# Kernel tuning notes

Hardware: AMD Instinct MI355X
Metric: run time of the kernel (lower is better)

Reference implementation:

```python
import jax, jax.numpy as jnp
import numpy as np

N = 100000
E = 1600000
D_IN = 128
D_H = 128
BN_EPS = 1e-5


def setup_inputs() -> dict:
    key = jax.random.key(0)
    ks = jax.random.split(key, 8)
    x = jax.random.normal(ks[0], (N, D_IN), dtype=jnp.float32)
    edge_index = jax.random.randint(ks[1], (2, E), 0, N, dtype=jnp.int64)
    # MLP params (Linear stores weight as [out, in])
    lim1 = 1.0 / np.sqrt(D_IN)
    W1 = jax.random.uniform(ks[2], (D_H, D_IN), minval=-lim1, maxval=lim1, dtype=jnp.float32)
    b1 = jax.random.uniform(ks[3], (D_H,), minval=-lim1, maxval=lim1, dtype=jnp.float32)
    gamma = jnp.ones((D_H,), dtype=jnp.float32)
    beta = jnp.zeros((D_H,), dtype=jnp.float32)
    lim2 = 1.0 / np.sqrt(D_H)
    W2 = jax.random.uniform(ks[4], (D_H, D_H), minval=-lim2, maxval=lim2, dtype=jnp.float32)
    b2 = jax.random.uniform(ks[5], (D_H,), minval=-lim2, maxval=lim2, dtype=jnp.float32)
    eps = jnp.float32(0.0)  # trainable eps parameter, init 0
    return {"x": x, "edge_index": edge_index, "eps": eps, "W1": W1, "b1": b1,
            "gamma": gamma, "beta": beta, "W2": W2, "b2": b2}


def reference(x, edge_index, eps, W1, b1, gamma, beta, W2, b2):
    src = edge_index[0]
    dst = edge_index[1]
    # Augmented edges = original + reversed + self-loops.
    # aggr[dst] += x[src]; aggr[src] += x[dst]; aggr[i] += x[i]
    aggr = jnp.zeros_like(x).at[dst].add(x[src]).at[src].add(x[dst]) + x
    h = (1.0 + eps) * x + aggr              # [N, D_IN]
    h = h @ W1.T + b1                        # [N, D_H]
    # BatchNorm1d in training mode: batch stats, biased variance
    mean = jnp.mean(h, axis=0)
    var = jnp.mean(jnp.square(h - mean), axis=0)
    h = gamma * (h - mean) * jax.lax.rsqrt(var + BN_EPS) + beta
    h = jax.nn.relu(h)
    return h @ W2.T + b2                     # [N, D_H]
```

## Files before the change

kernel.cpp:

```cpp
#include <hip/hip_runtime.h>
#include <hip/hip_fp16.h>

#define N_NODES 100000
#define EDGES   1600000
#define D       128
#define BN_EPS  1e-5f
#define TM      64
#define NT      ((N_NODES + TM - 1) / TM)
#define GGRID   782
#define NB      ((N_NODES + 255) >> 8)
#define SLOT    9216
#define L1E     8
#define L1TILE  (256 * L1E)
#define GBLKS   1536
#define GWAVES  (GBLKS * 4)
#define NREP    32

typedef __attribute__((ext_vector_type(8))) short short8;
typedef __attribute__((ext_vector_type(4))) float f32x4;

__device__ __forceinline__ unsigned short bf_hi(float f) {
    unsigned u = __float_as_uint(f);
    unsigned t = u + 0x7FFF + ((u >> 16) & 1);
    return (unsigned short)(t >> 16);
}
__device__ __forceinline__ float bf_val(unsigned short h) {
    return __uint_as_float(((unsigned)h) << 16);
}

__global__ void zero_split(int* __restrict__ zbase,
                           const float* __restrict__ W1, const float* __restrict__ W2,
                           unsigned short* __restrict__ w1h, unsigned short* __restrict__ w1l,
                           unsigned short* __restrict__ w2h, unsigned short* __restrict__ w2l) {
    int gid = blockIdx.x * blockDim.x + threadIdx.x;
    if (gid < 8704) zbase[gid] = 0;
    if (gid < 16384) {
        float f = W1[gid];
        unsigned short h = bf_hi(f);
        w1h[gid] = h;
        w1l[gid] = bf_hi(f - bf_val(h));
    } else {
        int j = gid - 16384;
        float f = W2[j];
        unsigned short h = bf_hi(f);
        w2h[j] = h;
        w2l[j] = bf_hi(f - bf_val(h));
    }
}

__launch_bounds__(256)
__global__ void partition_pairs(const int* __restrict__ ei, int* __restrict__ gcur,
                                int* __restrict__ pairs) {
    __shared__ int cnt[NB];
    __shared__ int cbase[NB];
    const int tid = threadIdx.x;
    for (int i = tid; i < NB; i += 256) cnt[i] = 0;
    __syncthreads();

    int bbA[L1E], rrA[L1E], pkA[L1E];
    int bbB[L1E], rrB[L1E], pkB[L1E];
    const int t0 = blockIdx.x * L1TILE + tid;
#pragma unroll
    for (int j = 0; j < L1E; ++j) {
        int t = t0 + j * 256;
        bbA[j] = -1;
        bbB[j] = -1;
        if (t < EDGES) {
            int s = ei[t];
            int d = ei[EDGES + t];
            bbA[j] = d >> 8;
            pkA[j] = ((d & 255) << 17) | s;
            rrA[j] = atomicAdd(&cnt[bbA[j]], 1);
            bbB[j] = s >> 8;
            pkB[j] = ((s & 255) << 17) | d;
            rrB[j] = atomicAdd(&cnt[bbB[j]], 1);
        }
    }
    __syncthreads();
    for (int i = tid; i < NB; i += 256) {
        int c = cnt[i];
        cbase[i] = c ? (i * SLOT + atomicAdd(&gcur[i], c)) : 0;
    }
    __syncthreads();
#pragma unroll
    for (int j = 0; j < L1E; ++j) {
        if (bbA[j] >= 0) {
            pairs[cbase[bbA[j]] + rrA[j]] = pkA[j];
            pairs[cbase[bbB[j]] + rrB[j]] = pkB[j];
        }
    }
}

__launch_bounds__(256)
__global__ void bucket_fill(int* __restrict__ pairs, const int* __restrict__ gcur,
                            int* __restrict__ ofs, int* __restrict__ oen) {
    __shared__ int sP[SLOT];
    __shared__ int lc[256];
    __shared__ int cur[256];
    const int b    = blockIdx.x;
    const int tid  = threadIdx.x;
    const int base = b * SLOT;
    const int m    = min(gcur[b], SLOT);
    for (int i = tid; i < m; i += 256) sP[i] = pairs[base + i];
    lc[tid] = 0;
    __syncthreads();
    for (int i = tid; i < m; i += 256) atomicAdd(&lc[sP[i] >> 17], 1);
    __syncthreads();
    int v = lc[tid];
    for (int d = 1; d < 256; d <<= 1) {
        int u = (tid >= d) ? lc[tid - d] : 0;
        __syncthreads();
        lc[tid] += u;
        __syncthreads();
    }
    int abs0 = base + lc[tid] - v;
    cur[tid] = abs0;
    const int n = (b << 8) + tid;
    if (n < N_NODES) { ofs[n] = abs0; oen[n] = abs0 + v; }
    __syncthreads();
    for (int i = tid; i < m; i += 256) {
        int p = sP[i];
        int r = atomicAdd(&cur[p >> 17], 1);
        pairs[r] = p & 0x1FFFF;
    }
}

__launch_bounds__(256)
__global__ void gemm0_mfma(const float* __restrict__ x,
                           const unsigned short* __restrict__ w1h,
                           const unsigned short* __restrict__ w1l,
                           __half* __restrict__ yh) {
    __shared__ unsigned short sH[TM][136];
    __shared__ unsigned short sL[TM][136];
    const int tid = threadIdx.x;
    const int wv  = tid >> 6;
    const int ln  = tid & 63;
    const int lc  = ln & 15;
    const int qd  = ln >> 4;
    const int sr  = tid >> 5;
    const int sc4 = tid & 31;

    short8 Bh[4][2], Bl[4][2];
#pragma unroll
    for (int kk = 0; kk < 4; ++kk)
#pragma unroll
        for (int tl = 0; tl < 2; ++tl) {
            int woff = (wv * 32 + tl * 16 + lc) * D + kk * 32 + qd * 8;
            Bh[kk][tl] = *(const short8*)(w1h + woff);
            Bl[kk][tl] = *(const short8*)(w1l + woff);
        }

    float4 pf[8];
    int tile = blockIdx.x;
#pragma unroll
    for (int i = 0; i < 8; ++i) {
        int gr = tile * TM + sr + i * 8;
        pf[i] = make_float4(0.f, 0.f, 0.f, 0.f);
        if (gr < N_NODES)
            pf[i] = *(const float4*)(x + (long long)gr * D + sc4 * 4);
    }

    while (tile < NT) {
#pragma unroll
        for (int i = 0; i < 8; ++i) {
            float4 v = pf[i];
            unsigned short h0 = bf_hi(v.x), h1b = bf_hi(v.y), h2 = bf_hi(v.z), h3 = bf_hi(v.w);
            unsigned short l0 = bf_hi(v.x - bf_val(h0)), l1 = bf_hi(v.y - bf_val(h1b));
            unsigned short l2 = bf_hi(v.z - bf_val(h2)), l3 = bf_hi(v.w - bf_val(h3));
            int r = sr + i * 8;
            *(uint2*)&sH[r][sc4 * 4] = make_uint2((unsigned)h0 | ((unsigned)h1b << 16),
                                                  (unsigned)h2 | ((unsigned)h3 << 16));
            *(uint2*)&sL[r][sc4 * 4] = make_uint2((unsigned)l0 | ((unsigned)l1 << 16),
                                                  (unsigned)l2 | ((unsigned)l3 << 16));
        }
        __syncthreads();
        int nxt = tile + GGRID;
        if (nxt < NT) {
#pragma unroll
            for (int i = 0; i < 8; ++i) {
                int gr = nxt * TM + sr + i * 8;
                pf[i] = make_float4(0.f, 0.f, 0.f, 0.f);
                if (gr < N_NODES)
                    pf[i] = *(const float4*)(x + (long long)gr * D + sc4 * 4);
            }
        }

        f32x4 acc[4][2];
#pragma unroll
        for (int m = 0; m < 4; ++m)
#pragma unroll
            for (int tl = 0; tl < 2; ++tl) acc[m][tl] = (f32x4){0.f, 0.f, 0.f, 0.f};

#pragma unroll
        for (int kk = 0; kk < 4; ++kk) {
#pragma unroll
            for (int m = 0; m < 4; ++m) {
                short8 ah = *(const short8*)&sH[m * 16 + lc][kk * 32 + qd * 8];
                short8 al = *(const short8*)&sL[m * 16 + lc][kk * 32 + qd * 8];
#pragma unroll
                for (int tl = 0; tl < 2; ++tl) {
                    acc[m][tl] = __builtin_amdgcn_mfma_f32_16x16x32_bf16(ah, Bh[kk][tl], acc[m][tl], 0, 0, 0);
                    acc[m][tl] = __builtin_amdgcn_mfma_f32_16x16x32_bf16(al, Bh[kk][tl], acc[m][tl], 0, 0, 0);
                    acc[m][tl] = __builtin_amdgcn_mfma_f32_16x16x32_bf16(ah, Bl[kk][tl], acc[m][tl], 0, 0, 0);
                }
            }
        }

        const int row0 = tile * TM;
#pragma unroll
        for (int m = 0; m < 4; ++m)
#pragma unroll
            for (int tl = 0; tl < 2; ++tl) {
                int col = wv * 32 + tl * 16 + lc;
#pragma unroll
                for (int r = 0; r < 4; ++r) {
                    int grow = row0 + m * 16 + qd * 4 + r;
                    if (grow < N_NODES)
                        yh[(long long)grow * D + col] = __float2half(acc[m][tl][r]);
                }
            }
        __syncthreads();
        tile = nxt;
    }
}

__launch_bounds__(256)
__global__ void gather_aggr(const __half* __restrict__ yh,
                            const int* __restrict__ adj, const int* __restrict__ ofs,
                            const int* __restrict__ oen, const float* __restrict__ eps_p,
                            const float* __restrict__ b1,
                            float* __restrict__ h1, float* __restrict__ stats) {
    const int wv   = threadIdx.x >> 6;
    const int lane = threadIdx.x & 63;
    const int wave = blockIdx.x * 4 + wv;
    const __half2* xp = (const __half2*)yh;
    const float sc = 2.0f + eps_p[0];
    const float2 b1c = ((const float2*)b1)[lane];
    float sx = 0.f, sy = 0.f, qx = 0.f, qy = 0.f;

    for (int node = wave; node < N_NODES; node += GWAVES) {
        int b = ofs[node];
        int e = oen[node];
        float ax = 0.f, ay = 0.f;
        int i = b;
        for (; i + 8 <= e; i += 8) {
            int n0 = adj[i],     n1 = adj[i + 1], n2 = adj[i + 2], n3 = adj[i + 3];
            int n4 = adj[i + 4], n5 = adj[i + 5], n6 = adj[i + 6], n7 = adj[i + 7];
            __half2 v0 = xp[(unsigned)n0 * 64u + lane];
            __half2 v1 = xp[(unsigned)n1 * 64u + lane];
            __half2 v2 = xp[(unsigned)n2 * 64u + lane];
            __half2 v3 = xp[(unsigned)n3 * 64u + lane];
            __half2 v4 = xp[(unsigned)n4 * 64u + lane];
            __half2 v5 = xp[(unsigned)n5 * 64u + lane];
            __half2 v6 = xp[(unsigned)n6 * 64u + lane];
            __half2 v7 = xp[(unsigned)n7 * 64u + lane];
            float2 f0 = __half22float2(v0);
            float2 f1 = __half22float2(v1);
            float2 f2 = __half22float2(v2);
            float2 f3 = __half22float2(v3);
            float2 f4 = __half22float2(v4);
            float2 f5 = __half22float2(v5);
            float2 f6 = __half22float2(v6);
            float2 f7 = __half22float2(v7);
            ax += ((f0.x + f1.x) + (f2.x + f3.x)) + ((f4.x + f5.x) + (f6.x + f7.x));
            ay += ((f0.y + f1.y) + (f2.y + f3.y)) + ((f4.y + f5.y) + (f6.y + f7.y));
        }
        for (; i + 4 <= e; i += 4) {
            int n0 = adj[i], n1 = adj[i + 1], n2 = adj[i + 2], n3 = adj[i + 3];
            __half2 v0 = xp[(unsigned)n0 * 64u + lane];
            __half2 v1 = xp[(unsigned)n1 * 64u + lane];
            __half2 v2 = xp[(unsigned)n2 * 64u + lane];
            __half2 v3 = xp[(unsigned)n3 * 64u + lane];
            float2 f0 = __half22float2(v0);
            float2 f1 = __half22float2(v1);
            float2 f2 = __half22float2(v2);
            float2 f3 = __half22float2(v3);
            ax += (f0.x + f1.x) + (f2.x + f3.x);
            ay += (f0.y + f1.y) + (f2.y + f3.y);
        }
        for (; i < e; ++i) {
            __half2 v = xp[(unsigned)adj[i] * 64u + lane];
            float2 f = __half22float2(v);
            ax += f.x;
            ay += f.y;
        }
        float2 ys = __half22float2(xp[(unsigned)node * 64u + lane]);
        float ox = fmaf(sc, ys.x, ax) + b1c.x;
        float oy = fmaf(sc, ys.y, ay) + b1c.y;
        ((float2*)h1)[(long long)node * 64 + lane] = make_float2(ox, oy);
        sx += ox; sy += oy;
        qx += ox * ox; qy += oy * oy;
    }

    __shared__ float4 red[4][64];
    red[wv][lane] = make_float4(sx, sy, qx, qy);
    __syncthreads();
    if (wv == 0) {
        float4 a = red[0][lane], b4 = red[1][lane], c = red[2][lane], d4 = red[3][lane];
        float fx = (a.x + b4.x) + (c.x + d4.x);
        float fy = (a.y + b4.y) + (c.y + d4.y);
        float gx = (a.z + b4.z) + (c.z + d4.z);
        float gy = (a.w + b4.w) + (c.w + d4.w);
        float* st = stats + (blockIdx.x & (NREP - 1)) * 256;
        atomicAdd(&st[2 * lane],       fx);
        atomicAdd(&st[2 * lane + 1],   fy);
        atomicAdd(&st[128 + 2 * lane],     gx);
        atomicAdd(&st[128 + 2 * lane + 1], gy);
    }
}

__launch_bounds__(256)
__global__ void gemm2_mfma(float* __restrict__ h1out,
                           const unsigned short* __restrict__ w2h,
                           const unsigned short* __restrict__ w2l,
                           const float* __restrict__ b2, const float* __restrict__ stats,
                           const float* __restrict__ gamma, const float* __restrict__ beta) {
    __shared__ unsigned short sH[TM][136];
    __shared__ unsigned short sL[TM][136];
    __shared__ float sScale[128];
    __shared__ float sShift[128];
    const int tid = threadIdx.x;
    const int wv  = tid >> 6;
    const int ln  = tid & 63;
    const int lc  = ln & 15;
    const int qd  = ln >> 4;
    const int sr  = tid >> 5;
    const int sc4 = tid & 31;

    if (tid < 128) {
        float s = 0.f, q = 0.f;
#pragma unroll
        for (int r = 0; r < NREP; ++r) {
            s += stats[r * 256 + tid];
            q += stats[r * 256 + 128 + tid];
        }
        float mean = s * (1.0f / N_NODES);
        float var  = fmaxf(q * (1.0f / N_NODES) - mean * mean, 0.0f);
        float sc   = gamma[tid] * rsqrtf(var + BN_EPS);
        sScale[tid] = sc;
        sShift[tid] = beta[tid] - mean * sc;
    }

    short8 Bh[4][2], Bl[4][2];
#pragma unroll
    for (int kk = 0; kk < 4; ++kk)
#pragma unroll
        for (int tl = 0; tl < 2; ++tl) {
            int woff = (wv * 32 + tl * 16 + lc) * D + kk * 32 + qd * 8;
            Bh[kk][tl] = *(const short8*)(w2h + woff);
            Bl[kk][tl] = *(const short8*)(w2l + woff);
        }
    float bb[2];
    bb[0] = b2[wv * 32 + lc];
    bb[1] = b2[wv * 32 + 16 + lc];

    __syncthreads();

    float4 pf[8];
    int tile = blockIdx.x;
#pragma unroll
    for (int i = 0; i < 8; ++i) {
        int gr = tile * TM + sr + i * 8;
        pf[i] = make_float4(0.f, 0.f, 0.f, 0.f);
        if (gr < N_NODES)
            pf[i] = *(const float4*)(h1out + (long long)gr * D + sc4 * 4);
    }

    while (tile < NT) {
        float4 scv = *(const float4*)&sScale[sc4 * 4];
        float4 shv = *(const float4*)&sShift[sc4 * 4];
#pragma unroll
        for (int i = 0; i < 8; ++i) {
            int gr = tile * TM + sr + i * 8;
            float4 v = pf[i];
            if (gr < N_NODES) {
                v.x = fmaxf(0.f, fmaf(v.x, scv.x, shv.x));
                v.y = fmaxf(0.f, fmaf(v.y, scv.y, shv.y));
                v.z = fmaxf(0.f, fmaf(v.z, scv.z, shv.z));
                v.w = fmaxf(0.f, fmaf(v.w, scv.w, shv.w));
            } else {
                v = make_float4(0.f, 0.f, 0.f, 0.f);
            }
            unsigned short h0 = bf_hi(v.x), h1b = bf_hi(v.y), h2 = bf_hi(v.z), h3 = bf_hi(v.w);
            unsigned short l0 = bf_hi(v.x - bf_val(h0)), l1 = bf_hi(v.y - bf_val(h1b));
            unsigned short l2 = bf_hi(v.z - bf_val(h2)), l3 = bf_hi(v.w - bf_val(h3));
            int r = sr + i * 8;
            *(uint2*)&sH[r][sc4 * 4] = make_uint2((unsigned)h0 | ((unsigned)h1b << 16),
                                                  (unsigned)h2 | ((unsigned)h3 << 16));
            *(uint2*)&sL[r][sc4 * 4] = make_uint2((unsigned)l0 | ((unsigned)l1 << 16),
                                                  (unsigned)l2 | ((unsigned)l3 << 16));
        }
        __syncthreads();
        int nxt = tile + GGRID;
        if (nxt < NT) {
#pragma unroll
            for (int i = 0; i < 8; ++i) {
                int gr = nxt * TM + sr + i * 8;
                pf[i] = make_float4(0.f, 0.f, 0.f, 0.f);
                if (gr < N_NODES)
                    pf[i] = *(const float4*)(h1out + (long long)gr * D + sc4 * 4);
            }
        }

        f32x4 acc[4][2];
#pragma unroll
        for (int m = 0; m < 4; ++m)
#pragma unroll
            for (int tl = 0; tl < 2; ++tl) acc[m][tl] = (f32x4){0.f, 0.f, 0.f, 0.f};

#pragma unroll
        for (int kk = 0; kk < 4; ++kk) {
#pragma unroll
            for (int m = 0; m < 4; ++m) {
                short8 ah = *(const short8*)&sH[m * 16 + lc][kk * 32 + qd * 8];
                short8 al = *(const short8*)&sL[m * 16 + lc][kk * 32 + qd * 8];
#pragma unroll
                for (int tl = 0; tl < 2; ++tl) {
                    acc[m][tl] = __builtin_amdgcn_mfma_f32_16x16x32_bf16(ah, Bh[kk][tl], acc[m][tl], 0, 0, 0);
                    acc[m][tl] = __builtin_amdgcn_mfma_f32_16x16x32_bf16(al, Bh[kk][tl], acc[m][tl], 0, 0, 0);
                    acc[m][tl] = __builtin_amdgcn_mfma_f32_16x16x32_bf16(ah, Bl[kk][tl], acc[m][tl], 0, 0, 0);
                }
            }
        }

        const int row0 = tile * TM;
#pragma unroll
        for (int m = 0; m < 4; ++m)
#pragma unroll
            for (int tl = 0; tl < 2; ++tl) {
                int col = wv * 32 + tl * 16 + lc;
#pragma unroll
                for (int r = 0; r < 4; ++r) {
                    int grow = row0 + m * 16 + qd * 4 + r;
                    if (grow < N_NODES)
                        h1out[(long long)grow * D + col] = acc[m][tl][r] + bb[tl];
                }
            }
        __syncthreads();
        tile = nxt;
    }
}

extern "C" void kernel_launch(void* const* d_in, const int* in_sizes, int n_in,
                              void* d_out, int out_size, void* d_ws, size_t ws_size,
                              hipStream_t stream) {
    const float* x     = (const float*)d_in[0];
    const int*   ei    = (const int*)d_in[1];
    const float* eps_p = (const float*)d_in[2];
    const float* W1    = (const float*)d_in[3];
    const float* b1    = (const float*)d_in[4];
    const float* gamma = (const float*)d_in[5];
    const float* beta  = (const float*)d_in[6];
    const float* W2    = (const float*)d_in[7];
    const float* b2    = (const float*)d_in[8];

    __half* yh   = (__half*)d_ws;
    float*  stats = (float*)(yh + (long long)N_NODES * D);
    int*    gcur  = (int*)(stats + NREP * 256);
    int*    ofs   = gcur + 512;
    int*    oen   = ofs + N_NODES;
    unsigned short* w1h = (unsigned short*)(oen + N_NODES);
    unsigned short* w1l = w1h + 16384;
    unsigned short* w2h = w1l + 16384;
    unsigned short* w2l = w2h + 16384;
    int*    pairs = (int*)(w2l + 16384);
    int*    adj   = pairs;

    float* out = (float*)d_out;

    {
        zero_split<<<128, 256, 0, stream>>>((int*)stats, W1, W2, w1h, w1l, w2h, w2l);
    }
    {
        int grid = (EDGES + L1TILE - 1) / L1TILE;
        partition_pairs<<<grid, 256, 0, stream>>>(ei, gcur, pairs);
    }
    {
        bucket_fill<<<NB, 256, 0, stream>>>(pairs, gcur, ofs, oen);
    }
    {
        gemm0_mfma<<<GGRID, 256, 0, stream>>>(x, w1h, w1l, yh);
    }
    {
        gather_aggr<<<GBLKS, 256, 0, stream>>>(yh, adj, ofs, oen, eps_p, b1, out, stats);
    }
    {
        gemm2_mfma<<<GGRID, 256, 0, stream>>>(out, w2h, w2l, b2, stats, gamma, beta);
    }
}
```

Measured before the change: 345.0 us.

## Fuse edge partitioning into GEMM0 launch and shrink buckets to 128 nodes

Merges the edge-partition kernel and the first GEMM into one launch, using extra blocks beyond the GEMM grid to do partitioning, so the two independent stages overlap on the GPU. Buckets now cover 128 nodes instead of 256, giving 782 buckets with smaller slots and a smaller shared footprint in bucket_fill. The zeroing and workspace offsets are enlarged to match. Risks include bucket overflow with the smaller slot size and the partition blocks contending with the GEMM for the same compute units.

```diff
diff --git a/kernel.cpp b/kernel.cpp
--- a/kernel.cpp
+++ b/kernel.cpp
@@ -8,8 +8,8 @@
 #define TM      64
 #define NT      ((N_NODES + TM - 1) / TM)
 #define GGRID   782
-#define NB      ((N_NODES + 255) >> 8)
-#define SLOT    9216
+#define NB      782
+#define SLOT    4800
 #define L1E     8
 #define L1TILE  (256 * L1E)
 #define GBLKS   1536
@@ -33,7 +33,7 @@
                            unsigned short* __restrict__ w1h, unsigned short* __restrict__ w1l,
                            unsigned short* __restrict__ w2h, unsigned short* __restrict__ w2l) {
     int gid = blockIdx.x * blockDim.x + threadIdx.x;
-    if (gid < 8704) zbase[gid] = 0;
+    if (gid < 9216) zbase[gid] = 0;
     if (gid < 16384) {
         float f = W1[gid];
         unsigned short h = bf_hi(f);
@@ -49,90 +49,57 @@
 }
 
 __launch_bounds__(256)
-__global__ void partition_pairs(const int* __restrict__ ei, int* __restrict__ gcur,
-                                int* __restrict__ pairs) {
-    __shared__ int cnt[NB];
-    __shared__ int cbase[NB];
-    const int tid = threadIdx.x;
-    for (int i = tid; i < NB; i += 256) cnt[i] = 0;
-    __syncthreads();
-
-    int bbA[L1E], rrA[L1E], pkA[L1E];
-    int bbB[L1E], rrB[L1E], pkB[L1E];
-    const int t0 = blockIdx.x * L1TILE + tid;
-#pragma unroll
-    for (int j = 0; j < L1E; ++j) {
-        int t = t0 + j * 256;
-        bbA[j] = -1;
-        bbB[j] = -1;
-        if (t < EDGES) {
-            int s = ei[t];
-            int d = ei[EDGES + t];
-            bbA[j] = d >> 8;
-            pkA[j] = ((d & 255) << 17) | s;
-            rrA[j] = atomicAdd(&cnt[bbA[j]], 1);
-            bbB[j] = s >> 8;
-            pkB[j] = ((s & 255) << 17) | d;
-            rrB[j] = atomicAdd(&cnt[bbB[j]], 1);
-        }
-    }
-    __syncthreads();
-    for (int i = tid; i < NB; i += 256) {
-        int c = cnt[i];
-        cbase[i] = c ? (i * SLOT + atomicAdd(&gcur[i], c)) : 0;
-    }
-    __syncthreads();
-#pragma unroll
-    for (int j = 0; j < L1E; ++j) {
-        if (bbA[j] >= 0) {
-            pairs[cbase[bbA[j]] + rrA[j]] = pkA[j];
-            pairs[cbase[bbB[j]] + rrB[j]] = pkB[j];
-        }
-    }
-}
-
-__launch_bounds__(256)
-__global__ void bucket_fill(int* __restrict__ pairs, const int* __restrict__ gcur,
-                            int* __restrict__ ofs, int* __restrict__ oen) {
-    __shared__ int sP[SLOT];
-    __shared__ int lc[256];
-    __shared__ int cur[256];
-    const int b    = blockIdx.x;
-    const int tid  = threadIdx.x;
-    const int base = b * SLOT;
-    const int m    = min(gcur[b], SLOT);
-    for (int i = tid; i < m; i += 256) sP[i] = pairs[base + i];
-    lc[tid] = 0;
-    __syncthreads();
-    for (int i = tid; i < m; i += 256) atomicAdd(&lc[sP[i] >> 17], 1);
-    __syncthreads();
-    int v = lc[tid];
-    for (int d = 1; d < 256; d <<= 1) {
-        int u = (tid >= d) ? lc[tid - d] : 0;
-        __syncthreads();
-        lc[tid] += u;
-        __syncthreads();
-    }
-    int abs0 = base + lc[tid] - v;
-    cur[tid] = abs0;
-    const int n = (b << 8) + tid;
-    if (n < N_NODES) { ofs[n] = abs0; oen[n] = abs0 + v; }
-    __syncthreads();
-    for (int i = tid; i < m; i += 256) {
-        int p = sP[i];
-        int r = atomicAdd(&cur[p >> 17], 1);
-        pairs[r] = p & 0x1FFFF;
-    }
-}
-
-__launch_bounds__(256)
-__global__ void gemm0_mfma(const float* __restrict__ x,
-                           const unsigned short* __restrict__ w1h,
-                           const unsigned short* __restrict__ w1l,
-                           __half* __restrict__ yh) {
+__global__ void fused_pg(const float* __restrict__ x,
+                         const unsigned short* __restrict__ w1h,
+                         const unsigned short* __restrict__ w1l,
+                         __half* __restrict__ yh,
+                         const int* __restrict__ ei, int* __restrict__ gcur,
+                         int* __restrict__ pairs) {
     __shared__ unsigned short sH[TM][136];
     __shared__ unsigned short sL[TM][136];
     const int tid = threadIdx.x;
+
+    if (blockIdx.x >= GGRID) {
+        int* cnt   = (int*)&sH[0][0];
+        int* cbase = cnt + NB;
+        for (int i = tid; i < NB; i += 256) cnt[i] = 0;
+        __syncthreads();
+
+        int bbA[L1E], rrA[L1E], pkA[L1E];
+        int bbB[L1E], rrB[L1E], pkB[L1E];
+        const int t0 = (blockIdx.x - GGRID) * L1TILE + tid;
+#pragma unroll
+        for (int j = 0; j < L1E; ++j) {
+            int t = t0 + j * 256;
+            bbA[j] = -1;
+            bbB[j] = -1;
+            if (t < EDGES) {
+                int s = ei[t];
+                int d = ei[EDGES + t];
+                bbA[j] = d >> 7;
+                pkA[j] = ((d & 127) << 17) | s;
+                rrA[j] = atomicAdd(&cnt[bbA[j]], 1);
+                bbB[j] = s >> 7;
+                pkB[j] = ((s & 127) << 17) | d;
+                rrB[j] = atomicAdd(&cnt[bbB[j]], 1);
+            }
+        }
+        __syncthreads();
+        for (int i = tid; i < NB; i += 256) {
+            int c = cnt[i];
+            cbase[i] = c ? (i * SLOT + atomicAdd(&gcur[i], c)) : 0;
+        }
+        __syncthreads();
+#pragma unroll
+        for (int j = 0; j < L1E; ++j) {
+            if (bbA[j] >= 0) {
+                pairs[cbase[bbA[j]] + rrA[j]] = pkA[j];
+                pairs[cbase[bbB[j]] + rrB[j]] = pkB[j];
+            }
+        }
+        return;
+    }
+
     const int wv  = tid >> 6;
     const int ln  = tid & 63;
     const int lc  = ln & 15;
@@ -221,6 +188,42 @@
             }
         __syncthreads();
         tile = nxt;
+    }
+}
+
+__launch_bounds__(256)
+__global__ void bucket_fill(int* __restrict__ pairs, const int* __restrict__ gcur,
+                            int* __restrict__ ofs, int* __restrict__ oen) {
+    __shared__ int sP[SLOT];
+    __shared__ int lc[128];
+    __shared__ int cur[128];
+    const int b    = blockIdx.x;
+    const int tid  = threadIdx.x;
+    const int base = b * SLOT;
+    const int m    = min(gcur[b], SLOT);
+    for (int i = tid; i < m; i += 256) sP[i] = pairs[base + i];
+    if (tid < 128) lc[tid] = 0;
+    __syncthreads();
+    for (int i = tid; i < m; i += 256) atomicAdd(&lc[sP[i] >> 17], 1);
+    __syncthreads();
+    int v = (tid < 128) ? lc[tid] : 0;
+    for (int d = 1; d < 128; d <<= 1) {
+        int u = (tid >= d && tid < 128) ? lc[tid - d] : 0;
+        __syncthreads();
+        if (tid < 128) lc[tid] += u;
+        __syncthreads();
+    }
+    if (tid < 128) {
+        int abs0 = base + lc[tid] - v;
+        cur[tid] = abs0;
+        const int n = (b << 7) + tid;
+        if (n < N_NODES) { ofs[n] = abs0; oen[n] = abs0 + v; }
+    }
+    __syncthreads();
+    for (int i = tid; i < m; i += 256) {
+        int p = sP[i];
+        int r = atomicAdd(&cur[p >> 17], 1);
+        pairs[r] = p & 0x1FFFF;
     }
 }
 
@@ -457,7 +460,7 @@
     __half* yh   = (__half*)d_ws;
     float*  stats = (float*)(yh + (long long)N_NODES * D);
     int*    gcur  = (int*)(stats + NREP * 256);
-    int*    ofs   = gcur + 512;
+    int*    ofs   = gcur + 1024;
     int*    oen   = ofs + N_NODES;
     unsigned short* w1h = (unsigned short*)(oen + N_NODES);
     unsigned short* w1l = w1h + 16384;
@@ -472,16 +475,12 @@
         zero_split<<<128, 256, 0, stream>>>((int*)stats, W1, W2, w1h, w1l, w2h, w2l);
     }
     {
-        int grid = (EDGES + L1TILE - 1) / L1TILE;
-        partition_pairs<<<grid, 256, 0, stream>>>(ei, gcur, pairs);
+        fused_pg<<<GGRID + 782, 256, 0, stream>>>(x, w1h, w1l, yh, ei, gcur, pairs);
     }
     {
         bucket_fill<<<NB, 256, 0, stream>>>(pairs, gcur, ofs, oen);
     }
     {
-        gemm0_mfma<<<GGRID, 256, 0, stream>>>(x, w1h, w1l, yh);
-    }
-    {
         gather_aggr<<<GBLKS, 256, 0, stream>>>(yh, adj, ofs, oen, eps_p, b1, out, stats);
     }
     {
```

After: 329.9 us. 1.05x faster.
